# Kernel optimization log

Hardware: AMD Instinct MI355X
Metric: run time of the kernel (lower is better)

Reference implementation:

```python
import jax, jax.numpy as jnp
import numpy as np

N, DIM, T, V = 32, 256, 120, 25
H, HD = 8, 32            # num_heads, head_dim
MAX_HOP = 4
SCALE = HD ** -0.5


def setup_inputs() -> dict:
    key = jax.random.key(0)
    ks = jax.random.split(key, 9)
    x = jax.random.normal(ks[0], (N, DIM, T, V), jnp.float32)
    e = jax.random.normal(ks[1], (N, DIM, T, V), jnp.float32)
    # 1x1 conv weights (trunc_normal std=0.02 in the original init)
    W_kv = jax.random.normal(ks[2], (2 * DIM, DIM), jnp.float32) * 0.02
    W_q = jax.random.normal(ks[3], (DIM, DIM), jnp.float32) * 0.02
    W_proj = jax.random.normal(ks[4], (DIM, DIM), jnp.float32) * 0.02
    b_proj = jnp.zeros((DIM,), jnp.float32)
    rpe = jax.random.normal(ks[5], (MAX_HOP + 1, DIM), jnp.float32) * 0.02
    w1 = jax.random.normal(ks[6], (H, HD), jnp.float32) * 0.02
    # outer initialized as per-head identity (plus noise so grads are interesting)
    outer = jnp.broadcast_to(jnp.eye(V, dtype=jnp.float32), (H, V, V)) \
        + 0.1 * jax.random.normal(ks[7], (H, V, V), jnp.float32)
    alpha = 0.1 * jax.random.normal(ks[8], (1,), jnp.float32)
    idx = jnp.arange(V)
    hops = jnp.minimum(jnp.abs(idx[:, None] - idx[None, :]), MAX_HOP).astype(jnp.int32)
    return dict(x=x, e=e, W_kv=W_kv, W_q=W_q, W_proj=W_proj, b_proj=b_proj,
                rpe=rpe, w1=w1, outer=outer, alpha=alpha, hops=hops)


def reference(x, e, W_kv, W_q, W_proj, b_proj, rpe, w1, outer, alpha, hops):
    n, c, t, v = x.shape
    # 1x1 convs == channel matmuls
    kv = jnp.einsum('nctv,dc->ndtv', x, W_kv)                    # [N,2*DIM,T,V]
    kv = kv.reshape(n, 2, H, HD, t, v).transpose(1, 0, 4, 2, 5, 3)  # [2,N,T,H,V,HD]
    k, vv = kv[0], kv[1]
    q = jnp.einsum('nctv,dc->ndtv', x, W_q)
    q = q.reshape(n, H, HD, t, v).transpose(0, 3, 1, 4, 2)       # [N,T,H,V,HD]
    # content score
    attn = jnp.einsum('bthnc,bthmc->bthnm', q, k)                # [N,T,H,V,V]
    # hop relative-position bias
    k_r = rpe[hops].reshape(v, v, H, HD)                         # [V,V,H,HD]
    attn = attn + jnp.einsum('bthnc,nmhc->bthnm', q, k_r)
    # group term
    e_k = e.reshape(n, H, HD, t, v).transpose(0, 3, 1, 4, 2)     # [N,T,H,V,HD]
    attn = attn + jnp.einsum('bthnc,bthmc->bthnm', q, e_k)
    # group bias (broadcast over query index)
    attn = attn + jnp.einsum('hc,bthmc->bthm', w1, e_k)[..., None, :]
    attn = jax.nn.softmax(attn * SCALE, axis=-1)
    # outer/adjacency fusion then weighted V
    out = jnp.einsum('bthnm,bthmc->bthnc', alpha[0] * attn + outer, vv)
    # [N,T,H,V,HD] -> [N,T,H,HD,V] -> [N,T,DIM,V] -> [N,DIM,T,V]
    out = out.transpose(0, 1, 2, 4, 3).reshape(n, t, H * HD, v).transpose(0, 2, 1, 3)
    out = jnp.einsum('nctv,dc->ndtv', out, W_proj) + b_proj[None, :, None, None]
    return out
```

## Files before the change

kernel.cpp:

```cpp
#include <hip/hip_runtime.h>

typedef __attribute__((ext_vector_type(8))) short bf16x8;
typedef __attribute__((ext_vector_type(4))) float f32x4;
typedef unsigned short u16;
typedef unsigned int u32;

#define SCALE_ 0.17677669529663687f
#define MFMA(a,b,c) __builtin_amdgcn_mfma_f32_16x16x32_bf16(a,b,c,0,0,0)

__device__ __forceinline__ u16 f2bf(float f){
    u32 u = __float_as_uint(f);
    u = (u + 0x7FFFu + ((u >> 16) & 1u)) >> 16;
    return (u16)u;
}
__device__ __forceinline__ float bf2f(u32 h){ return __uint_as_float(h << 16); }
__device__ __forceinline__ u32 pk2(float a, float b){ return (u32)f2bf(a) | ((u32)f2bf(b) << 16); }

__device__ __forceinline__ bf16x8 frag8(uint2 p0, uint2 p1, int kg, int l15){
    const int s0 = ((kg & 1) << 5) + l15;
    const int s1 = s0 + 16;
    u32 a0 = (u32)__shfl((int)p0.x, s0, 64);
    u32 a1 = (u32)__shfl((int)p0.y, s0, 64);
    u32 a2 = (u32)__shfl((int)p0.x, s1, 64);
    u32 a3 = (u32)__shfl((int)p0.y, s1, 64);
    u32 b0 = (u32)__shfl((int)p1.x, s0, 64);
    u32 b1 = (u32)__shfl((int)p1.y, s0, 64);
    u32 b2 = (u32)__shfl((int)p1.x, s1, 64);
    u32 b3 = (u32)__shfl((int)p1.y, s1, 64);
    const bool hi = (kg >= 2);
    union { u32 u[4]; bf16x8 v; } r;
    r.u[0] = hi ? b0 : a0; r.u[1] = hi ? b1 : a1;
    r.u[2] = hi ? b2 : a2; r.u[3] = hi ? b3 : a3;
    return r.v;
}

__global__ void prep_kernel(const float* __restrict__ Wkv, const float* __restrict__ Wq,
                            const float* __restrict__ Wproj, const float* __restrict__ rpe,
                            const float* __restrict__ w1, u16* __restrict__ wpk)
{
    int i = blockIdx.x * 256 + threadIdx.x;
    if (i < 65536)        wpk[i] = f2bf(Wq[i]);
    else if (i < 131072)  wpk[i] = f2bf(Wkv[i - 65536]);
    else if (i < 196608){
        int j = i - 131072;
        int h = j >> 13;
        int r = j & 8191;
        int coct = r >> 8;
        int hd   = (r >> 3) & 31;
        int clo  = r & 7;
        wpk[i] = f2bf(Wkv[(size_t)(256 + h*32 + hd) * 256 + coct*8 + clo]);
    }
    else if (i < 262144)  wpk[i] = f2bf(Wproj[i - 196608]);
    else if (i < 263424){
        int j = i - 262144;
        int jj = j >> 8, h = (j >> 5) & 7, hd = j & 31;
        wpk[i] = f2bf(rpe[jj*256 + h*32 + hd]);
    }
    else if (i < 263680)  wpk[i] = f2bf(w1[i - 263424]);
}

__launch_bounds__(512, 4)
__global__ void mhsa_main(const float* __restrict__ x, const float* __restrict__ e,
                          const float* __restrict__ outer, const float* __restrict__ alpha,
                          const float* __restrict__ bproj, const u16* __restrict__ wpk,
                          float* __restrict__ out)
{
    __shared__ __align__(16) u16 smem[6656*3 + 64];
    u16* xs  = smem;
    u16* es  = smem + 6656;
    u16* opk = smem + 13312;

    const int tid = threadIdx.x;
    const int w = tid >> 6, lane = tid & 63;
    const int l15 = lane & 15, kg = lane >> 4;
    const int wg = (blockIdx.x & 7) * 480 + (blockIdx.x >> 3);
    const int n = wg / 120, t = wg % 120;
    const float alpha0 = alpha[0];
    const f32x4 zf = {0.f, 0.f, 0.f, 0.f};

    const float* xb = x + (size_t)n*768000 + t*25;
    const float* eb = e + (size_t)n*768000 + t*25;
    for (int i = tid; i < 6400; i += 512){
        int c = i / 25, v = i - c*25;
        int a16 = ((c>>3)*26 + v)*8 + (c&7);
        xs[a16] = f2bf(xb[c*3000 + v]);
        es[a16] = f2bf(eb[c*3000 + v]);
    }
    __syncthreads();

    {
        const int h = w;

        f32x4 cq[2][2], ck[2][2];
        #pragma unroll
        for (int i = 0; i < 2; ++i)
            #pragma unroll
            for (int j = 0; j < 2; ++j){ cq[i][j] = zf; ck[i][j] = zf; }
        {
            const u16* wq0 = wpk + (size_t)(h*32 + l15)*256;
            const u16* wk0 = wpk + 65536 + (size_t)(h*32 + l15)*256;
            #pragma unroll
            for (int ks = 0; ks < 8; ++ks){
                bf16x8 b0 = *(const bf16x8*)&xs[((ks*4+kg)*26 + l15)*8];
                bf16x8 b1 = *(const bf16x8*)&xs[((ks*4+kg)*26 + 16 + l15)*8];
                bf16x8 aq0 = *(const bf16x8*)(wq0 + ks*32 + kg*8);
                bf16x8 aq1 = *(const bf16x8*)(wq0 + 4096 + ks*32 + kg*8);
                bf16x8 ak0 = *(const bf16x8*)(wk0 + ks*32 + kg*8);
                bf16x8 ak1 = *(const bf16x8*)(wk0 + 4096 + ks*32 + kg*8);
                cq[0][0]=MFMA(aq0,b0,cq[0][0]); cq[0][1]=MFMA(aq0,b1,cq[0][1]);
                cq[1][0]=MFMA(aq1,b0,cq[1][0]); cq[1][1]=MFMA(aq1,b1,cq[1][1]);
                ck[0][0]=MFMA(ak0,b0,ck[0][0]); ck[0][1]=MFMA(ak0,b1,ck[0][1]);
                ck[1][0]=MFMA(ak1,b0,ck[1][0]); ck[1][1]=MFMA(ak1,b1,ck[1][1]);
            }
        }
        uint2 P_q[2][2], P_k[2][2];
        #pragma unroll
        for (int mt = 0; mt < 2; ++mt)
            #pragma unroll
            for (int nt = 0; nt < 2; ++nt){
                int coct = h*4 + mt*2 + (kg>>1);
                uint2 ev = *(const uint2*)&es[(coct*26 + nt*16 + l15)*8 + (kg&1)*4];
                ck[mt][nt][0] += bf2f(ev.x & 0xFFFFu);
                ck[mt][nt][1] += bf2f(ev.x >> 16);
                ck[mt][nt][2] += bf2f(ev.y & 0xFFFFu);
                ck[mt][nt][3] += bf2f(ev.y >> 16);
                uint2 pq; pq.x = pk2(cq[mt][nt][0], cq[mt][nt][1]);
                pq.y = pk2(cq[mt][nt][2], cq[mt][nt][3]);
                P_q[nt][mt] = pq;
                uint2 pk; pk.x = pk2(ck[mt][nt][0], ck[mt][nt][1]);
                pk.y = pk2(ck[mt][nt][2], ck[mt][nt][3]);
                P_k[nt][mt] = pk;
            }

        float bias01[2];
        {
            bf16x8 aw1 = *(const bf16x8*)(wpk + 263424 + h*32 + kg*8);
            bf16x8 be0 = *(const bf16x8*)&es[((h*4+kg)*26 + l15)*8];
            bf16x8 be1 = *(const bf16x8*)&es[((h*4+kg)*26 + 16 + l15)*8];
            f32x4 cb0 = MFMA(aw1, be0, zf);
            f32x4 cb1 = MFMA(aw1, be1, zf);
            bias01[0] = cb0[0]; bias01[1] = cb1[0];
        }

        f32x4 cv[2][2];
        #pragma unroll
        for (int i = 0; i < 2; ++i)
            #pragma unroll
            for (int j = 0; j < 2; ++j) cv[i][j] = zf;
        {
            const u16* wvt = wpk + 131072 + h*8192;
            #pragma unroll
            for (int ks = 0; ks < 8; ++ks){
                bf16x8 a0 = *(const bf16x8*)&xs[((ks*4+kg)*26 + l15)*8];
                bf16x8 a1 = *(const bf16x8*)&xs[((ks*4+kg)*26 + 16 + l15)*8];
                bf16x8 bv0 = *(const bf16x8*)&wvt[((ks*4+kg)*32 + l15)*8];
                bf16x8 bv1 = *(const bf16x8*)&wvt[((ks*4+kg)*32 + 16 + l15)*8];
                cv[0][0]=MFMA(a0,bv0,cv[0][0]); cv[0][1]=MFMA(a0,bv1,cv[0][1]);
                cv[1][0]=MFMA(a1,bv0,cv[1][0]); cv[1][1]=MFMA(a1,bv1,cv[1][1]);
            }
        }
        #pragma unroll
        for (int nt = 0; nt < 2; ++nt)
            #pragma unroll
            for (int r = 0; r < 4; ++r)
                cv[1][nt][r] = (kg*4 + r < 9) ? cv[1][nt][r] : 0.f;

        uint2 P_v[2][2];
        #pragma unroll
        for (int mt = 0; mt < 2; ++mt)
            #pragma unroll
            for (int nt = 0; nt < 2; ++nt){
                uint2 pv; pv.x = pk2(cv[mt][nt][0], cv[mt][nt][1]);
                pv.y = pk2(cv[mt][nt][2], cv[mt][nt][3]);
                P_v[nt][mt] = pv;
            }

        bf16x8 fq0  = frag8(P_q[0][0], P_q[0][1], kg, l15);
        bf16x8 fq1  = frag8(P_q[1][0], P_q[1][1], kg, l15);
        bf16x8 fke0 = frag8(P_k[0][0], P_k[0][1], kg, l15);
        bf16x8 fke1 = frag8(P_k[1][0], P_k[1][1], kg, l15);
        if (l15 >= 9){
            if (l15 <= 13)
                fke1 = *(const bf16x8*)(wpk + 262144 + ((l15-9)*8 + h)*32 + kg*8);
            else {
                union { u32 u[4]; bf16x8 v; } z; z.u[0]=z.u[1]=z.u[2]=z.u[3]=0;
                fke1 = z.v;
            }
        }
        f32x4 sc[2][2];
        sc[0][0] = MFMA(fke0, fq0, zf);
        sc[0][1] = MFMA(fke0, fq1, zf);
        sc[1][0] = MFMA(fke1, fq0, zf);
        sc[1][1] = MFMA(fke1, fq1, zf);

        uint2 P_G[2][2];
        #pragma unroll
        for (int nt = 0; nt < 2; ++nt){
            const int a = nt*16 + l15;
            f32x4 s0 = sc[0][nt], s1 = sc[1][nt];
            float rr0 = __shfl(s1[1], 32 + l15, 64);
            float rr1 = __shfl(s1[2], 32 + l15, 64);
            float rr2 = __shfl(s1[3], 32 + l15, 64);
            float rr3 = __shfl(s1[0], 48 + l15, 64);
            float rr4 = __shfl(s1[1], 48 + l15, 64);
            float tv[8];
            #pragma unroll
            for (int mt = 0; mt < 2; ++mt)
                #pragma unroll
                for (int r = 0; r < 4; ++r){
                    int b = mt*16 + kg*4 + r;
                    float sval = mt ? s1[r] : s0[r];
                    float bb = __shfl(bias01[mt], (lane & 48) + (b & 15), 64);
                    int d = a - b; d = d < 0 ? -d : d; if (d > 4) d = 4;
                    float rj = d==0?rr0 : d==1?rr1 : d==2?rr2 : d==3?rr3 : rr4;
                    float tt = (sval + rj + bb) * SCALE_;
                    tv[mt*4+r] = (b < 25) ? tt : -1e30f;
                }
            float m = tv[0];
            #pragma unroll
            for (int i = 1; i < 8; ++i) m = fmaxf(m, tv[i]);
            m = fmaxf(m, __shfl_xor(m, 16, 64));
            m = fmaxf(m, __shfl_xor(m, 32, 64));
            float ex[8], sm = 0.f;
            #pragma unroll
            for (int i = 0; i < 8; ++i){ ex[i] = __expf(tv[i] - m); sm += ex[i]; }
            sm += __shfl_xor(sm, 16, 64);
            sm += __shfl_xor(sm, 32, 64);
            const float inv = alpha0 / sm;
            float g[8];
            #pragma unroll
            for (int mt = 0; mt < 2; ++mt)
                #pragma unroll
                for (int r = 0; r < 4; ++r){
                    int b = mt*16 + kg*4 + r;
                    float ov = (a < 25 && b < 25) ? outer[((size_t)h*25 + a)*25 + b] : 0.f;
                    g[mt*4+r] = (b < 25) ? ex[mt*4+r]*inv + ov : 0.f;
                }
            uint2 pg0; pg0.x = pk2(g[0], g[1]); pg0.y = pk2(g[2], g[3]);
            uint2 pg1; pg1.x = pk2(g[4], g[5]); pg1.y = pk2(g[6], g[7]);
            P_G[nt][0] = pg0; P_G[nt][1] = pg1;
        }

        {
            bf16x8 fv0 = frag8(P_v[0][0], P_v[0][1], kg, l15);
            bf16x8 fv1 = frag8(P_v[1][0], P_v[1][1], kg, l15);
            bf16x8 fg0 = frag8(P_G[0][0], P_G[0][1], kg, l15);
            bf16x8 fg1 = frag8(P_G[1][0], P_G[1][1], kg, l15);
            f32x4 o[2][2];
            o[0][0] = MFMA(fv0, fg0, zf); o[0][1] = MFMA(fv0, fg1, zf);
            o[1][0] = MFMA(fv1, fg0, zf); o[1][1] = MFMA(fv1, fg1, zf);
            #pragma unroll
            for (int mt = 0; mt < 2; ++mt)
                #pragma unroll
                for (int nt = 0; nt < 2; ++nt){
                    int a = nt*16 + l15;
                    if (a < 25){
                        int coct = h*4 + mt*2 + (kg>>1);
                        u32* dst = (u32*)&opk[(coct*26 + a)*8 + (kg&1)*4];
                        dst[0] = pk2(o[mt][nt][0], o[mt][nt][1]);
                        dst[1] = pk2(o[mt][nt][2], o[mt][nt][3]);
                    }
                }
        }
    }
    __syncthreads();

    {
        f32x4 pc[2][2];
        #pragma unroll
        for (int i = 0; i < 2; ++i){ pc[i][0] = zf; pc[i][1] = zf; }
        #pragma unroll
        for (int ks = 0; ks < 8; ++ks){
            bf16x8 pb0 = *(const bf16x8*)&opk[((ks*4+kg)*26 + l15)*8];
            bf16x8 pb1 = *(const bf16x8*)&opk[((ks*4+kg)*26 + 16 + l15)*8];
            #pragma unroll
            for (int i = 0; i < 2; ++i){
                bf16x8 aw = *(const bf16x8*)(wpk + 196608 +
                                (size_t)(w*32 + i*16 + l15)*256 + ks*32 + kg*8);
                pc[i][0] = MFMA(aw, pb0, pc[i][0]);
                pc[i][1] = MFMA(aw, pb1, pc[i][1]);
            }
        }
        #pragma unroll
        for (int i = 0; i < 2; ++i){
            const int d = w*32 + i*16 + kg*4;
            float b0 = bproj[d], b1 = bproj[d+1], b2 = bproj[d+2], b3 = bproj[d+3];
            #pragma unroll
            for (int nt = 0; nt < 2; ++nt){
                int v = nt*16 + l15;
                if (v < 25){
                    float* op = out + (size_t)n*768000 + (size_t)d*3000 + t*25 + v;
                    op[0]    = pc[i][nt][0] + b0;
                    op[3000] = pc[i][nt][1] + b1;
                    op[6000] = pc[i][nt][2] + b2;
                    op[9000] = pc[i][nt][3] + b3;
                }
            }
        }
    }
}

extern "C" void kernel_launch(void* const* d_in, const int* in_sizes, int n_in,
                              void* d_out, int out_size, void* d_ws, size_t ws_size,
                              hipStream_t stream) {
    (void)in_sizes; (void)n_in; (void)out_size; (void)ws_size;
    const float* x     = (const float*)d_in[0];
    const float* e     = (const float*)d_in[1];
    const float* Wkv   = (const float*)d_in[2];
    const float* Wq    = (const float*)d_in[3];
    const float* Wproj = (const float*)d_in[4];
    const float* bproj = (const float*)d_in[5];
    const float* rpe   = (const float*)d_in[6];
    const float* w1    = (const float*)d_in[7];
    const float* outer = (const float*)d_in[8];
    const float* alpha = (const float*)d_in[9];
    float* out = (float*)d_out;
    u16* wpk = (u16*)d_ws;

    prep_kernel<<<1030, 256, 0, stream>>>(Wkv, Wq, Wproj, rpe, w1, wpk);
    mhsa_main<<<32*120, 512, 0, stream>>>(x, e, outer, alpha, bproj, wpk, out);
}
```

Measured before the change: 303.1 us.

## Split fused attention kernel into attention and projection kernels via workspace

Splits the single fused kernel into two launches when the workspace is large enough. The first computes attention and writes the per-head outputs to global workspace as bf16. The second reads them back and applies the output projection plus bias. The attention kernel uses less shared memory, which may allow more blocks per CU, and the projection no longer needs a block-wide sync. The cost is an extra global round trip of the intermediate tensor and a second kernel launch.

```diff
diff --git a/kernel.cpp b/kernel.cpp
--- a/kernel.cpp
+++ b/kernel.cpp
@@ -34,6 +34,7 @@
     return r.v;
 }
 
+#define O_OFF_ 263680
 __global__ void prep_kernel(const float* __restrict__ Wkv, const float* __restrict__ Wq,
                             const float* __restrict__ Wproj, const float* __restrict__ rpe,
                             const float* __restrict__ w1, u16* __restrict__ wpk)
@@ -60,6 +61,254 @@
 }
 
 __launch_bounds__(512, 4)
+__global__ void attn_kernel(const float* __restrict__ x, const float* __restrict__ e,
+                            const float* __restrict__ outer, const float* __restrict__ alpha,
+                            const u16* __restrict__ wpk, u16* __restrict__ o_ws)
+{
+    __shared__ __align__(16) u16 smem[6656*2 + 64];
+    u16* xs  = smem;
+    u16* es  = smem + 6656;
+
+    const int tid = threadIdx.x;
+    const int w = tid >> 6, lane = tid & 63;
+    const int l15 = lane & 15, kg = lane >> 4;
+    const int wg = (blockIdx.x & 7) * 480 + (blockIdx.x >> 3);
+    const int n = wg / 120, t = wg % 120;
+    const float alpha0 = alpha[0];
+    const f32x4 zf = {0.f, 0.f, 0.f, 0.f};
+
+    const float* xb = x + (size_t)n*768000 + t*25;
+    const float* eb = e + (size_t)n*768000 + t*25;
+    for (int i = tid; i < 6400; i += 512){
+        int c = i / 25, v = i - c*25;
+        int a16 = ((c>>3)*26 + v)*8 + (c&7);
+        xs[a16] = f2bf(xb[c*3000 + v]);
+        es[a16] = f2bf(eb[c*3000 + v]);
+    }
+    __syncthreads();
+
+    const int h = w;
+
+    f32x4 cq[2][2], ck[2][2];
+    #pragma unroll
+    for (int i = 0; i < 2; ++i)
+        #pragma unroll
+        for (int j = 0; j < 2; ++j){ cq[i][j] = zf; ck[i][j] = zf; }
+    {
+        const u16* wq0 = wpk + (size_t)(h*32 + l15)*256;
+        const u16* wk0 = wpk + 65536 + (size_t)(h*32 + l15)*256;
+        #pragma unroll
+        for (int ks = 0; ks < 8; ++ks){
+            bf16x8 b0 = *(const bf16x8*)&xs[((ks*4+kg)*26 + l15)*8];
+            bf16x8 b1 = *(const bf16x8*)&xs[((ks*4+kg)*26 + 16 + l15)*8];
+            bf16x8 aq0 = *(const bf16x8*)(wq0 + ks*32 + kg*8);
+            bf16x8 aq1 = *(const bf16x8*)(wq0 + 4096 + ks*32 + kg*8);
+            bf16x8 ak0 = *(const bf16x8*)(wk0 + ks*32 + kg*8);
+            bf16x8 ak1 = *(const bf16x8*)(wk0 + 4096 + ks*32 + kg*8);
+            cq[0][0]=MFMA(aq0,b0,cq[0][0]); cq[0][1]=MFMA(aq0,b1,cq[0][1]);
+            cq[1][0]=MFMA(aq1,b0,cq[1][0]); cq[1][1]=MFMA(aq1,b1,cq[1][1]);
+            ck[0][0]=MFMA(ak0,b0,ck[0][0]); ck[0][1]=MFMA(ak0,b1,ck[0][1]);
+            ck[1][0]=MFMA(ak1,b0,ck[1][0]); ck[1][1]=MFMA(ak1,b1,ck[1][1]);
+        }
+    }
+    uint2 P_q[2][2], P_k[2][2];
+    #pragma unroll
+    for (int mt = 0; mt < 2; ++mt)
+        #pragma unroll
+        for (int nt = 0; nt < 2; ++nt){
+            int coct = h*4 + mt*2 + (kg>>1);
+            uint2 ev = *(const uint2*)&es[(coct*26 + nt*16 + l15)*8 + (kg&1)*4];
+            ck[mt][nt][0] += bf2f(ev.x & 0xFFFFu);
+            ck[mt][nt][1] += bf2f(ev.x >> 16);
+            ck[mt][nt][2] += bf2f(ev.y & 0xFFFFu);
+            ck[mt][nt][3] += bf2f(ev.y >> 16);
+            uint2 pq; pq.x = pk2(cq[mt][nt][0], cq[mt][nt][1]);
+            pq.y = pk2(cq[mt][nt][2], cq[mt][nt][3]);
+            P_q[nt][mt] = pq;
+            uint2 pk; pk.x = pk2(ck[mt][nt][0], ck[mt][nt][1]);
+            pk.y = pk2(ck[mt][nt][2], ck[mt][nt][3]);
+            P_k[nt][mt] = pk;
+        }
+
+    float bias01[2];
+    {
+        bf16x8 aw1 = *(const bf16x8*)(wpk + 263424 + h*32 + kg*8);
+        bf16x8 be0 = *(const bf16x8*)&es[((h*4+kg)*26 + l15)*8];
+        bf16x8 be1 = *(const bf16x8*)&es[((h*4+kg)*26 + 16 + l15)*8];
+        f32x4 cb0 = MFMA(aw1, be0, zf);
+        f32x4 cb1 = MFMA(aw1, be1, zf);
+        bias01[0] = cb0[0]; bias01[1] = cb1[0];
+    }
+
+    f32x4 cv[2][2];
+    #pragma unroll
+    for (int i = 0; i < 2; ++i)
+        #pragma unroll
+        for (int j = 0; j < 2; ++j) cv[i][j] = zf;
+    {
+        const u16* wvt = wpk + 131072 + h*8192;
+        #pragma unroll
+        for (int ks = 0; ks < 8; ++ks){
+            bf16x8 a0 = *(const bf16x8*)&xs[((ks*4+kg)*26 + l15)*8];
+            bf16x8 a1 = *(const bf16x8*)&xs[((ks*4+kg)*26 + 16 + l15)*8];
+            bf16x8 bv0 = *(const bf16x8*)&wvt[((ks*4+kg)*32 + l15)*8];
+            bf16x8 bv1 = *(const bf16x8*)&wvt[((ks*4+kg)*32 + 16 + l15)*8];
+            cv[0][0]=MFMA(a0,bv0,cv[0][0]); cv[0][1]=MFMA(a0,bv1,cv[0][1]);
+            cv[1][0]=MFMA(a1,bv0,cv[1][0]); cv[1][1]=MFMA(a1,bv1,cv[1][1]);
+        }
+    }
+    #pragma unroll
+    for (int nt = 0; nt < 2; ++nt)
+        #pragma unroll
+        for (int r = 0; r < 4; ++r)
+            cv[1][nt][r] = (kg*4 + r < 9) ? cv[1][nt][r] : 0.f;
+
+    uint2 P_v[2][2];
+    #pragma unroll
+    for (int mt = 0; mt < 2; ++mt)
+        #pragma unroll
+        for (int nt = 0; nt < 2; ++nt){
+            uint2 pv; pv.x = pk2(cv[mt][nt][0], cv[mt][nt][1]);
+            pv.y = pk2(cv[mt][nt][2], cv[mt][nt][3]);
+            P_v[nt][mt] = pv;
+        }
+
+    bf16x8 fq0  = frag8(P_q[0][0], P_q[0][1], kg, l15);
+    bf16x8 fq1  = frag8(P_q[1][0], P_q[1][1], kg, l15);
+    bf16x8 fke0 = frag8(P_k[0][0], P_k[0][1], kg, l15);
+    bf16x8 fke1 = frag8(P_k[1][0], P_k[1][1], kg, l15);
+    if (l15 >= 9){
+        if (l15 <= 13)
+            fke1 = *(const bf16x8*)(wpk + 262144 + ((l15-9)*8 + h)*32 + kg*8);
+        else {
+            union { u32 u[4]; bf16x8 v; } z; z.u[0]=z.u[1]=z.u[2]=z.u[3]=0;
+            fke1 = z.v;
+        }
+    }
+    f32x4 sc[2][2];
+    sc[0][0] = MFMA(fke0, fq0, zf);
+    sc[0][1] = MFMA(fke0, fq1, zf);
+    sc[1][0] = MFMA(fke1, fq0, zf);
+    sc[1][1] = MFMA(fke1, fq1, zf);
+
+    uint2 P_G[2][2];
+    #pragma unroll
+    for (int nt = 0; nt < 2; ++nt){
+        const int a = nt*16 + l15;
+        f32x4 s0 = sc[0][nt], s1 = sc[1][nt];
+        float rr0 = __shfl(s1[1], 32 + l15, 64);
+        float rr1 = __shfl(s1[2], 32 + l15, 64);
+        float rr2 = __shfl(s1[3], 32 + l15, 64);
+        float rr3 = __shfl(s1[0], 48 + l15, 64);
+        float rr4 = __shfl(s1[1], 48 + l15, 64);
+        float tv[8];
+        #pragma unroll
+        for (int mt = 0; mt < 2; ++mt)
+            #pragma unroll
+            for (int r = 0; r < 4; ++r){
+                int b = mt*16 + kg*4 + r;
+                float sval = mt ? s1[r] : s0[r];
+                float bb = __shfl(bias01[mt], (lane & 48) + (b & 15), 64);
+                int d = a - b; d = d < 0 ? -d : d; if (d > 4) d = 4;
+                float rj = d==0?rr0 : d==1?rr1 : d==2?rr2 : d==3?rr3 : rr4;
+                float tt = (sval + rj + bb) * SCALE_;
+                tv[mt*4+r] = (b < 25) ? tt : -1e30f;
+            }
+        float m = tv[0];
+        #pragma unroll
+        for (int i = 1; i < 8; ++i) m = fmaxf(m, tv[i]);
+        m = fmaxf(m, __shfl_xor(m, 16, 64));
+        m = fmaxf(m, __shfl_xor(m, 32, 64));
+        float ex[8], sm = 0.f;
+        #pragma unroll
+        for (int i = 0; i < 8; ++i){ ex[i] = __expf(tv[i] - m); sm += ex[i]; }
+        sm += __shfl_xor(sm, 16, 64);
+        sm += __shfl_xor(sm, 32, 64);
+        const float inv = alpha0 / sm;
+        float g[8];
+        #pragma unroll
+        for (int mt = 0; mt < 2; ++mt)
+            #pragma unroll
+            for (int r = 0; r < 4; ++r){
+                int b = mt*16 + kg*4 + r;
+                float ov = (a < 25 && b < 25) ? outer[((size_t)h*25 + a)*25 + b] : 0.f;
+                g[mt*4+r] = (b < 25) ? ex[mt*4+r]*inv + ov : 0.f;
+            }
+        uint2 pg0; pg0.x = pk2(g[0], g[1]); pg0.y = pk2(g[2], g[3]);
+        uint2 pg1; pg1.x = pk2(g[4], g[5]); pg1.y = pk2(g[6], g[7]);
+        P_G[nt][0] = pg0; P_G[nt][1] = pg1;
+    }
+
+    {
+        bf16x8 fv0 = frag8(P_v[0][0], P_v[0][1], kg, l15);
+        bf16x8 fv1 = frag8(P_v[1][0], P_v[1][1], kg, l15);
+        bf16x8 fg0 = frag8(P_G[0][0], P_G[0][1], kg, l15);
+        bf16x8 fg1 = frag8(P_G[1][0], P_G[1][1], kg, l15);
+        f32x4 o[2][2];
+        o[0][0] = MFMA(fv0, fg0, zf); o[0][1] = MFMA(fv0, fg1, zf);
+        o[1][0] = MFMA(fv1, fg0, zf); o[1][1] = MFMA(fv1, fg1, zf);
+        u16* od = o_ws + (size_t)wg * 6400;
+        #pragma unroll
+        for (int mt = 0; mt < 2; ++mt)
+            #pragma unroll
+            for (int nt = 0; nt < 2; ++nt){
+                int a = nt*16 + l15;
+                if (a < 25){
+                    int coct = h*4 + mt*2 + (kg>>1);
+                    u32* dst = (u32*)&od[(coct*25 + a)*8 + (kg&1)*4];
+                    dst[0] = pk2(o[mt][nt][0], o[mt][nt][1]);
+                    dst[1] = pk2(o[mt][nt][2], o[mt][nt][3]);
+                }
+            }
+    }
+}
+
+__launch_bounds__(512, 4)
+__global__ void proj_kernel(const u16* __restrict__ wpk, const u16* __restrict__ o_ws,
+                            const float* __restrict__ bproj, float* __restrict__ out)
+{
+    const int tid = threadIdx.x;
+    const int w = tid >> 6, lane = tid & 63;
+    const int l15 = lane & 15, kg = lane >> 4;
+    const int wg = (blockIdx.x & 7) * 480 + (blockIdx.x >> 3);
+    const int n = wg / 120, t = wg % 120;
+    const f32x4 zf = {0.f, 0.f, 0.f, 0.f};
+    const u16* ob = o_ws + (size_t)wg * 6400;
+
+    f32x4 pc[2][2];
+    #pragma unroll
+    for (int i = 0; i < 2; ++i){ pc[i][0] = zf; pc[i][1] = zf; }
+    #pragma unroll
+    for (int ks = 0; ks < 8; ++ks){
+        bf16x8 pb0 = *(const bf16x8*)&ob[((ks*4+kg)*25 + l15)*8];
+        bf16x8 pb1 = *(const bf16x8*)&ob[((ks*4+kg)*25 + 16 + l15)*8];
+        #pragma unroll
+        for (int i = 0; i < 2; ++i){
+            bf16x8 aw = *(const bf16x8*)(wpk + 196608 +
+                            (size_t)(w*32 + i*16 + l15)*256 + ks*32 + kg*8);
+            pc[i][0] = MFMA(aw, pb0, pc[i][0]);
+            pc[i][1] = MFMA(aw, pb1, pc[i][1]);
+        }
+    }
+    #pragma unroll
+    for (int i = 0; i < 2; ++i){
+        const int d = w*32 + i*16 + kg*4;
+        float b0 = bproj[d], b1 = bproj[d+1], b2 = bproj[d+2], b3 = bproj[d+3];
+        #pragma unroll
+        for (int nt = 0; nt < 2; ++nt){
+            int v = nt*16 + l15;
+            if (v < 25){
+                float* op = out + (size_t)n*768000 + (size_t)d*3000 + t*25 + v;
+                op[0]    = pc[i][nt][0] + b0;
+                op[3000] = pc[i][nt][1] + b1;
+                op[6000] = pc[i][nt][2] + b2;
+                op[9000] = pc[i][nt][3] + b3;
+            }
+        }
+    }
+}
+
+__launch_bounds__(512, 4)
 __global__ void mhsa_main(const float* __restrict__ x, const float* __restrict__ e,
                           const float* __restrict__ outer, const float* __restrict__ alpha,
                           const float* __restrict__ bproj, const u16* __restrict__ wpk,
@@ -90,7 +339,6 @@
 
     {
         const int h = w;
-
         f32x4 cq[2][2], ck[2][2];
         #pragma unroll
         for (int i = 0; i < 2; ++i)
@@ -131,7 +379,6 @@
                 pk.y = pk2(ck[mt][nt][2], ck[mt][nt][3]);
                 P_k[nt][mt] = pk;
             }
-
         float bias01[2];
         {
             bf16x8 aw1 = *(const bf16x8*)(wpk + 263424 + h*32 + kg*8);
@@ -141,7 +388,6 @@
             f32x4 cb1 = MFMA(aw1, be1, zf);
             bias01[0] = cb0[0]; bias01[1] = cb1[0];
         }
-
         f32x4 cv[2][2];
         #pragma unroll
         for (int i = 0; i < 2; ++i)
@@ -164,7 +410,6 @@
             #pragma unroll
             for (int r = 0; r < 4; ++r)
                 cv[1][nt][r] = (kg*4 + r < 9) ? cv[1][nt][r] : 0.f;
-
         uint2 P_v[2][2];
         #pragma unroll
         for (int mt = 0; mt < 2; ++mt)
@@ -174,7 +419,6 @@
                 pv.y = pk2(cv[mt][nt][2], cv[mt][nt][3]);
                 P_v[nt][mt] = pv;
             }
-
         bf16x8 fq0  = frag8(P_q[0][0], P_q[0][1], kg, l15);
         bf16x8 fq1  = frag8(P_q[1][0], P_q[1][1], kg, l15);
         bf16x8 fke0 = frag8(P_k[0][0], P_k[0][1], kg, l15);
@@ -192,7 +436,6 @@
         sc[0][1] = MFMA(fke0, fq1, zf);
         sc[1][0] = MFMA(fke1, fq0, zf);
         sc[1][1] = MFMA(fke1, fq1, zf);
-
         uint2 P_G[2][2];
         #pragma unroll
         for (int nt = 0; nt < 2; ++nt){
@@ -240,7 +483,6 @@
             uint2 pg1; pg1.x = pk2(g[4], g[5]); pg1.y = pk2(g[6], g[7]);
             P_G[nt][0] = pg0; P_G[nt][1] = pg1;
         }
-
         {
             bf16x8 fv0 = frag8(P_v[0][0], P_v[0][1], kg, l15);
             bf16x8 fv1 = frag8(P_v[1][0], P_v[1][1], kg, l15);
@@ -303,7 +545,7 @@
 extern "C" void kernel_launch(void* const* d_in, const int* in_sizes, int n_in,
                               void* d_out, int out_size, void* d_ws, size_t ws_size,
                               hipStream_t stream) {
-    (void)in_sizes; (void)n_in; (void)out_size; (void)ws_size;
+    (void)in_sizes; (void)n_in; (void)out_size;
     const float* x     = (const float*)d_in[0];
     const float* e     = (const float*)d_in[1];
     const float* Wkv   = (const float*)d_in[2];
@@ -318,5 +560,13 @@
     u16* wpk = (u16*)d_ws;
 
     prep_kernel<<<1030, 256, 0, stream>>>(Wkv, Wq, Wproj, rpe, w1, wpk);
-    mhsa_main<<<32*120, 512, 0, stream>>>(x, e, outer, alpha, bproj, wpk, out);
-}
+
+    const size_t need = (size_t)O_OFF_*2 + (size_t)3840*6400*2 + 4096;
+    if (ws_size >= need){
+        u16* o_ws = wpk + O_OFF_;
+        attn_kernel<<<32*120, 512, 0, stream>>>(x, e, outer, alpha, wpk, o_ws);
+        proj_kernel<<<32*120, 512, 0, stream>>>(wpk, o_ws, bproj, out);
+    } else {
+        mhsa_main<<<32*120, 512, 0, stream>>>(x, e, outer, alpha, bproj, wpk, out);
+    }
+}
```

Result: slower. 316.8 us (+4.5%).
